# Kernel tuning notes

Measured on AMD Instinct MI355X. Metric: run time of the kernel, lower is better.

Reference implementation:

```python
import jax, jax.numpy as jnp
import numpy as np

BETA = 0.25  # commitment cost


def setup_inputs() -> dict:
    key = jax.random.key(0)
    k1, k2 = jax.random.split(key)
    z = jax.random.normal(k1, (16, 512, 64, 64), dtype=jnp.float32)       # (B, C=e_dim, H, W)
    codebook = jax.random.normal(k2, (1024, 512), dtype=jnp.float32)      # (n_e, e_dim)
    return {"z": z, "codebook": codebook}


def reference(z, codebook):
    b, c, h, w = z.shape
    zp = jnp.transpose(z, (0, 2, 3, 1))                                   # (B, H, W, C)
    zf = zp.reshape(-1, c)                                                # (N, e_dim)

    d = (jnp.sum(zf * zf, axis=1, keepdims=True)
         + jnp.sum(codebook * codebook, axis=1)
         - 2.0 * (zf @ codebook.T))                                       # (N, n_e)
    idx = jnp.argmin(d, axis=1)                                           # (N,)

    # one-hot @ codebook == direct gather
    z_q = codebook[idx].reshape(zp.shape)                                 # (B, H, W, C)

    sg = jax.lax.stop_gradient
    e_latent_loss = jnp.mean((sg(z_q) - zp) ** 2)
    q_latent_loss = jnp.mean((z_q - sg(zp)) ** 2)
    codebook_loss = q_latent_loss + BETA * e_latent_loss

    # straight-through estimator
    z_q_st = zp + sg(z_q - zp)
    z_q_out = jnp.transpose(z_q_st, (0, 3, 1, 2))                         # (B, C, H, W)
    return z_q_out, codebook_loss, idx.reshape(b, 1, h, w)
```

## Files before the change

### kernel.cpp

```cpp
#include <hip/hip_runtime.h>
#include <hip/hip_bf16.h>


typedef _Float16 h8 __attribute__((ext_vector_type(8)));
typedef float f32x16 __attribute__((ext_vector_type(16)));

#define OUT_LOSS  33554432
#define OUT_IDX   33554433
#define MARGIN_T  0.15f

__device__ __forceinline__ void gload_lds16(const void* g, void* l) {
  __builtin_amdgcn_global_load_lds(
      (const __attribute__((address_space(1))) void*)g,
      (__attribute__((address_space(3))) void*)l, 16, 0, 0);
}

__device__ __forceinline__ int zswz(int row) {
  return ((row & 3) << 6) | (((row >> 2) & 3) << 4);
}

__global__ __launch_bounds__(64) void k0_prep(
    const float* __restrict__ cb, unsigned short* __restrict__ cbT,
    float* __restrict__ cnp, int* __restrict__ counters, float* __restrict__ loss_acc,
    int* __restrict__ idx_ws, unsigned long long* __restrict__ packed_ws)
{
  const int r = blockIdx.x, l = threadIdx.x;
  const float* row = cb + (size_t)r * 512;
  float4 a  = *(const float4*)(row + l * 8);
  float4 b4 = *(const float4*)(row + l * 8 + 4);
  h8 hv;
  hv[0] = (_Float16)a.x;  hv[1] = (_Float16)a.y;  hv[2] = (_Float16)a.z;  hv[3] = (_Float16)a.w;
  hv[4] = (_Float16)b4.x; hv[5] = (_Float16)b4.y; hv[6] = (_Float16)b4.z; hv[7] = (_Float16)b4.w;
  {
    const int c  = r >> 5, rr = r & 31;
    const int s  = l >> 1;
    const int hk = l & 1;
    char* dst = reinterpret_cast<char*>(cbT)
              + (size_t)(c * 32 + s) * 1024 + (hk * 32 + rr) * 16;
    *reinterpret_cast<h8*>(dst) = hv;
  }
  float s = a.x*a.x + a.y*a.y + a.z*a.z + a.w*a.w
          + b4.x*b4.x + b4.y*b4.y + b4.z*b4.z + b4.w*b4.w;
  #pragma unroll
  for (int off = 1; off < 64; off <<= 1) s += __shfl_xor(s, off);
  if (l == 0) {
    int jr = r & 31, c = r >> 5;
    int khalf = (jr >> 2) & 1;
    int pat = jr - (khalf << 2);
    int rr2 = (pat & 3) + ((pat >> 3) << 2);
    cnp[(c << 5) + (khalf << 4) + rr2] = 0.5f * s;
  }
  const int pix = (r << 6) + l;
  idx_ws[pix] = (int)0x80000000;
  packed_ws[pix] = ~0ull;
  if (r == 0 && l < 4) counters[l] = 0;
  if (r == 0 && l == 0) *loss_acc = 0.f;
}

__global__ __launch_bounds__(256, 2) void k1_main(
    const float* __restrict__ z, const unsigned short* __restrict__ cbT,
    const float* __restrict__ cnp,
    int* __restrict__ idx_ws, int* __restrict__ flaglist,
    unsigned long long* __restrict__ pairlist, int* __restrict__ counters)
{
  extern __shared__ char smem[];
  float* cn_lds = reinterpret_cast<float*>(smem + 49152);
  const int tid   = threadIdx.x;
  const int lane  = tid & 63;
  const int wave  = tid >> 6;
  const int pxl   = lane & 31;
  const int khalf = lane >> 5;
  const int px0   = blockIdx.x << 7;
  const int b     = px0 >> 12;
  const int hw0   = px0 & 4095;
  const char* cbB = reinterpret_cast<const char*>(cbT);

  h8 bfrag[32];
  for (int i = tid; i < 1024; i += 256) cn_lds[i] = cnp[i];
  #pragma unroll
  for (int p = 0; p < 4; ++p) {
    #pragma unroll
    for (int it2 = 0; it2 < 2; ++it2) {
      const int cg  = tid >> 5;
      const int ch0 = it2 * 64 + cg * 8;
      const int pq  = (tid & 31) * 4;
      const float* src = z + ((size_t)(b * 512 + p * 128 + ch0)) * 4096 + hw0 + pq;
      float4 v[8];
      #pragma unroll
      for (int j = 0; j < 8; ++j) v[j] = *(const float4*)(src + (size_t)j * 4096);
      const float* vf = reinterpret_cast<const float*>(v);
      #pragma unroll
      for (int dp = 0; dp < 4; ++dp) {
        h8 hv;
        #pragma unroll
        for (int j = 0; j < 8; ++j) hv[j] = (_Float16)vf[j * 4 + dp];
        int row = pq + dp;
        int a = (row << 8) + ch0 * 2;
        a ^= zswz(row);
        *reinterpret_cast<h8*>(smem + a) = hv;
      }
    }
    __syncthreads();
    {
      const int row  = (wave << 5) + pxl;
      const int sw   = zswz(row);
      const int base = (row << 8) + (khalf << 4);
      #pragma unroll
      for (int ss = 0; ss < 8; ++ss)
        bfrag[p * 8 + ss] = *reinterpret_cast<const h8*>(smem + ((base + (ss << 5)) ^ sw));
    }
    __syncthreads();
  }

  #pragma unroll
  for (int i = 0; i < 4; ++i)
    gload_lds16(cbB + tid * 16 + i * 4096, smem + tid * 16 + i * 4096);
  #pragma unroll
  for (int i = 0; i < 4; ++i)
    gload_lds16(cbB + 16384 + tid * 16 + i * 4096, smem + 16384 + tid * 16 + i * 4096);
  __syncthreads();

  float v0 = INFINITY, v1 = INFINITY, v2 = INFINITY, v3 = INFINITY;
  int   i0 = 0, i1 = 0, i2 = 0, i3 = 0;
  f32x16 acca, accb;
  #pragma unroll
  for (int i = 0; i < 16; ++i) { acca[i] = 0.f; accb[i] = 0.f; }

  char* p0 = smem;
  char* p1 = smem + 16384;
  char* p2 = smem + 32768;

  for (int c = 0; c < 32; ++c) {
    const bool pf = (c < 31);
    asm volatile("s_waitcnt vmcnt(4)" ::: "memory");
    __builtin_amdgcn_s_barrier();
    __builtin_amdgcn_sched_barrier(0);
    if (pf) {
      const char* src = cbB + (c + 1) * 32768 + tid * 16;
      #pragma unroll
      for (int i = 0; i < 4; ++i)
        gload_lds16(src + i * 4096, p2 + tid * 16 + i * 4096);
    }
    {
      const char* ab = p0 + (khalf << 9) + (pxl << 4);
      h8 f[16];
      #pragma unroll
      for (int q = 0; q < 16; ++q) f[q] = *reinterpret_cast<const h8*>(ab + (q << 10));
      __builtin_amdgcn_s_setprio(1);
      #pragma unroll
      for (int q = 0; q < 8; ++q) {
        acca = __builtin_amdgcn_mfma_f32_32x32x16_f16(f[q],     bfrag[q],     acca, 0, 0, 0);
        accb = __builtin_amdgcn_mfma_f32_32x32x16_f16(f[q + 8], bfrag[q + 8], accb, 0, 0, 0);
      }
      __builtin_amdgcn_s_setprio(0);
    }
    { char* t = p0; p0 = p1; p1 = p2; p2 = t; }
    if (pf) { asm volatile("s_waitcnt vmcnt(4)" ::: "memory"); }
    else    { asm volatile("s_waitcnt vmcnt(0)" ::: "memory"); }
    __builtin_amdgcn_s_barrier();
    __builtin_amdgcn_sched_barrier(0);
    if (pf) {
      const char* src = cbB + (c + 1) * 32768 + 16384 + tid * 16;
      #pragma unroll
      for (int i = 0; i < 4; ++i)
        gload_lds16(src + i * 4096, p2 + tid * 16 + i * 4096);
    }
    {
      const char* ab = p0 + (khalf << 9) + (pxl << 4);
      h8 f[16];
      #pragma unroll
      for (int q = 0; q < 16; ++q) f[q] = *reinterpret_cast<const h8*>(ab + (q << 10));
      __builtin_amdgcn_s_setprio(1);
      #pragma unroll
      for (int q = 0; q < 8; ++q) {
        acca = __builtin_amdgcn_mfma_f32_32x32x16_f16(f[q],     bfrag[16 + q], acca, 0, 0, 0);
        accb = __builtin_amdgcn_mfma_f32_32x32x16_f16(f[q + 8], bfrag[24 + q], accb, 0, 0, 0);
      }
      __builtin_amdgcn_s_setprio(0);
    }
    { char* t = p0; p0 = p1; p1 = p2; p2 = t; }

    {
      const float* cl = cn_lds + (c << 5) + (khalf << 4);
      float4 q0 = *(const float4*)(cl);     float4 q1 = *(const float4*)(cl + 4);
      float4 q2 = *(const float4*)(cl + 8); float4 q3 = *(const float4*)(cl + 12);
      const float cn[16] = {q0.x,q0.y,q0.z,q0.w, q1.x,q1.y,q1.z,q1.w,
                            q2.x,q2.y,q2.z,q2.w, q3.x,q3.y,q3.z,q3.w};
      float sc[16];
      #pragma unroll
      for (int r = 0; r < 16; ++r) sc[r] = cn[r] - (acca[r] + accb[r]);
      float mn = sc[0];
      #pragma unroll
      for (int r = 1; r < 16; ++r) mn = fminf(mn, sc[r]);
      if (__ballot(mn < v3)) {
        const int jbase = (c << 5) + (khalf << 2);
        #pragma unroll
        for (int r = 0; r < 16; ++r) {
          int j = jbase + ((r & 3) + ((r >> 2) << 3));
          float s = sc[r];
          bool c0 = s < v0, c1 = s < v1, c2 = s < v2, c3 = s < v3;
          v3 = c2 ? v2 : (c3 ? s : v3);  i3 = c2 ? i2 : (c3 ? j : i3);
          v2 = c1 ? v1 : (c2 ? s : v2);  i2 = c1 ? i1 : (c2 ? j : i2);
          v1 = c0 ? v0 : (c1 ? s : v1);  i1 = c0 ? i0 : (c1 ? j : i1);
          v0 = c0 ? s  : v0;             i0 = c0 ? j  : i0;
        }
      }
      #pragma unroll
      for (int i = 0; i < 16; ++i) { acca[i] = 0.f; accb[i] = 0.f; }
    }
  }

  {
    float ow0 = __shfl_xor(v0, 32), ow1 = __shfl_xor(v1, 32),
          ow2 = __shfl_xor(v2, 32), ow3 = __shfl_xor(v3, 32);
    int   oj0 = __shfl_xor(i0, 32), oj1 = __shfl_xor(i1, 32),
          oj2 = __shfl_xor(i2, 32), oj3 = __shfl_xor(i3, 32);
    const float ow[4] = {ow0, ow1, ow2, ow3};
    const int   oj[4] = {oj0, oj1, oj2, oj3};
    #pragma unroll
    for (int k = 0; k < 4; ++k) {
      float ov = ow[k]; int oi = oj[k];
      bool c0 = ov < v0, c1 = ov < v1, c2 = ov < v2, c3 = ov < v3;
      v3 = c2 ? v2 : (c3 ? ov : v3);  i3 = c2 ? i2 : (c3 ? oi : i3);
      v2 = c1 ? v1 : (c2 ? ov : v2);  i2 = c1 ? i1 : (c2 ? oi : i2);
      v1 = c0 ? v0 : (c1 ? ov : v1);  i1 = c0 ? i0 : (c1 ? oi : i1);
      v0 = c0 ? ov : v0;              i0 = c0 ? oi : i0;
    }
  }

  const int pix = px0 + (wave << 5) + lane;
  bool sane = (v0 == v0) && (v3 == v3) && ((unsigned)i0 < 1024u);
  bool unfl = sane && (v1 - v0 >= MARGIN_T);
  bool quad = sane && !unfl && (v3 - v0 >= MARGIN_T);
  bool qpred = (lane < 32) && quad;
  bool fpred = (lane < 32) && !unfl && !quad;
  if (lane < 32) idx_ws[pix] = unfl ? i0 : (int)0x80000000;

  unsigned long long qm = __ballot(qpred);
  if (qm) {
    int leader = __ffsll(qm) - 1;
    int base = 0;
    if (lane == leader) base = atomicAdd(&counters[1], __popcll(qm));
    base = __shfl(base, leader);
    if (qpred) {
      int pos = __popcll(qm & ((1ull << lane) - 1ull));
      pairlist[base + pos] = (unsigned long long)(unsigned)pix
          | ((unsigned long long)(unsigned)i0 << 16)
          | ((unsigned long long)(unsigned)i1 << 26)
          | ((unsigned long long)(unsigned)i2 << 36)
          | ((unsigned long long)(unsigned)i3 << 46);
    }
  }
  unsigned long long fm = __ballot(fpred);
  if (fm) {
    int leader = __ffsll(fm) - 1;
    int base = 0;
    if (lane == leader) base = atomicAdd(&counters[0], __popcll(fm));
    base = __shfl(base, leader);
    if (fpred) {
      int pos = __popcll(fm & ((1ull << lane) - 1ull));
      flaglist[base + pos] = pix;
    }
  }
}

__global__ __launch_bounds__(256) void k2a_quad(
    const float* __restrict__ z, const float* __restrict__ cb,
    const unsigned long long* __restrict__ pairlist, const int* __restrict__ counters,
    int* __restrict__ idx_ws)
{
  const int lane = threadIdx.x & 63;
  const int wid  = (blockIdx.x << 2) + (threadIdx.x >> 6);
  const int nwav = gridDim.x << 2;
  const int nf   = counters[1];
  for (int e = wid; e < nf; e += nwav) {
    unsigned long long pk = pairlist[e];
    int pix = (int)(pk & 0xFFFFull);
    int c0 = (int)((pk >> 16) & 1023ull), c1 = (int)((pk >> 26) & 1023ull);
    int c2 = (int)((pk >> 36) & 1023ull), c3 = (int)((pk >> 46) & 1023ull);
    const float* zp = z + (size_t)(pix >> 12) * 512 * 4096 + (pix & 4095);
    double s0 = 0, s1 = 0, s2 = 0, s3 = 0;
    #pragma unroll
    for (int k = 0; k < 8; ++k) {
      int c = lane + (k << 6);
      double zv2 = 2.0 * (double)zp[(size_t)c * 4096];
      double a;
      a = (double)cb[(size_t)c0 * 512 + c]; s0 = fma(a, a - zv2, s0);
      a = (double)cb[(size_t)c1 * 512 + c]; s1 = fma(a, a - zv2, s1);
      a = (double)cb[(size_t)c2 * 512 + c]; s2 = fma(a, a - zv2, s2);
      a = (double)cb[(size_t)c3 * 512 + c]; s3 = fma(a, a - zv2, s3);
    }
    #pragma unroll
    for (int off = 32; off > 0; off >>= 1) {
      s0 += __shfl_xor(s0, off); s1 += __shfl_xor(s1, off);
      s2 += __shfl_xor(s2, off); s3 += __shfl_xor(s3, off);
    }
    double bv = s0; int bi = c0;
    if (s1 < bv || (s1 == bv && c1 < bi)) { bv = s1; bi = c1; }
    if (s2 < bv || (s2 == bv && c2 < bi)) { bv = s2; bi = c2; }
    if (s3 < bv || (s3 == bv && c3 < bi)) { bv = s3; bi = c3; }
    if (lane == 0) idx_ws[pix] = bi;
  }
}

__global__ __launch_bounds__(256) void k2_rescan(
    const float* __restrict__ z, const float* __restrict__ cb,
    const int* __restrict__ flaglist, const int* __restrict__ counters,
    unsigned long long* __restrict__ packed_ws)
{
  __shared__ float zb[16][512];
  __shared__ unsigned long long best[16];
  __shared__ int pixl[16];
  const int t = threadIdx.x;
  const int nflag = counters[0];
  const int ntasks = ((nflag + 15) >> 4) << 2;
  for (int task = blockIdx.x; task < ntasks; task += gridDim.x) {
    const int g = task >> 2, q = task & 3;
    int rem = nflag - (g << 4);
    const int npx = rem < 16 ? rem : 16;
    if (t < 16) {
      best[t] = ~0ull;
      pixl[t] = (t < npx) ? flaglist[(g << 4) + t] : 0;
    }
    __syncthreads();
    for (int i = t; i < (npx << 9); i += 256) {
      int p = i >> 9, c = i & 511;
      int pix = pixl[p];
      zb[p][c] = z[((size_t)(pix >> 12) * 512 + c) * 4096 + (pix & 4095)];
    }
    __syncthreads();
    const int j = (q << 8) + t;
    const float* row = cb + (size_t)j * 512;
    double dot[16];
    #pragma unroll
    for (int p = 0; p < 16; ++p) dot[p] = 0.0;
    double cn = 0.0;
    for (int k = 0; k < 512; k += 4) {
      float4 cv = *(const float4*)(row + k);
      double c0 = cv.x, c1 = cv.y, c2 = cv.z, c3 = cv.w;
      cn = fma(c0, c0, cn); cn = fma(c1, c1, cn);
      cn = fma(c2, c2, cn); cn = fma(c3, c3, cn);
      #pragma unroll
      for (int p = 0; p < 16; ++p) {
        dot[p] = fma(c0, (double)zb[p][k + 0], dot[p]);
        dot[p] = fma(c1, (double)zb[p][k + 1], dot[p]);
        dot[p] = fma(c2, (double)zb[p][k + 2], dot[p]);
        dot[p] = fma(c3, (double)zb[p][k + 3], dot[p]);
      }
    }
    #pragma unroll
    for (int p = 0; p < 16; ++p) {
      if (p < npx) {
        double d = fma(-2.0, dot[p], cn);
        unsigned long long u = (unsigned long long)__double_as_longlong(d);
        u = (u >> 63) ? ~u : (u | 0x8000000000000000ull);
        unsigned long long pkk = (u & ~1023ull) | (unsigned long long)j;
        atomicMin(&best[p], pkk);
      }
    }
    __syncthreads();
    if (t < npx) atomicMin(&packed_ws[pixl[t]], best[t]);
    __syncthreads();
  }
}

__global__ __launch_bounds__(256) void k3_out(
    const float* __restrict__ z, const float* __restrict__ cb,
    const int* __restrict__ idx_ws, const unsigned long long* __restrict__ packed_ws,
    float* __restrict__ out, float* __restrict__ loss_acc)
{
  extern __shared__ float rows[];
  __shared__ int idxs[32];
  __shared__ float wsum[4];
  const int t = threadIdx.x;
  const int pix0 = blockIdx.x << 5;
  const int b = pix0 >> 12, hw0 = pix0 & 4095;
  if (t < 32) {
    int pix = pix0 + t;
    int v = idx_ws[pix];
    unsigned j = (v < 0) ? (unsigned)(packed_ws[pix] & 1023ull) : (unsigned)v;
    j &= 1023u;
    idxs[t] = (int)j;
    out[OUT_IDX + pix] = (float)j;
  }
  __syncthreads();
  for (int i = t; i < 32 * 128; i += 256) {
    int r = i >> 7, kq = (i & 127) << 2;
    float4 v = *(const float4*)(cb + (size_t)idxs[r] * 512 + kq);
    float* dst = rows + r * 513 + kq;
    dst[0] = v.x; dst[1] = v.y; dst[2] = v.z; dst[3] = v.w;
  }
  __syncthreads();
  const int pl = (t & 7) << 2;
  const int cg = t >> 3;
  float acc = 0.f;
  for (int c0 = 0; c0 < 512; c0 += 32) {
    int c = c0 + cg;
    size_t go = ((size_t)(b * 512 + c)) * 4096 + hw0 + pl;
    float4 zv = *(const float4*)(z + go);
    float q0 = rows[(pl + 0) * 513 + c], q1 = rows[(pl + 1) * 513 + c];
    float q2 = rows[(pl + 2) * 513 + c], q3 = rows[(pl + 3) * 513 + c];
    float d0 = q0 - zv.x, d1 = q1 - zv.y, d2 = q2 - zv.z, d3 = q3 - zv.w;
    acc = fmaf(d0, d0, acc); acc = fmaf(d1, d1, acc);
    acc = fmaf(d2, d2, acc); acc = fmaf(d3, d3, acc);
    float4 qv;
    qv.x = zv.x + d0; qv.y = zv.y + d1;
    qv.z = zv.z + d2; qv.w = zv.w + d3;
    *reinterpret_cast<float4*>(out + go) = qv;
  }
  #pragma unroll
  for (int off = 32; off > 0; off >>= 1) acc += __shfl_down(acc, off);
  if ((t & 63) == 0) wsum[t >> 6] = acc;
  __syncthreads();
  if (t == 0) atomicAdd(loss_acc, wsum[0] + wsum[1] + wsum[2] + wsum[3]);
}

__global__ void k4_loss(const float* __restrict__ loss_acc, float* __restrict__ out)
{
  if (threadIdx.x == 0 && blockIdx.x == 0)
    out[OUT_LOSS] = loss_acc[0] * (1.25f / 33554432.f);
}

extern "C" void kernel_launch(void* const* d_in, const int* in_sizes, int n_in,
                              void* d_out, int out_size, void* d_ws, size_t ws_size,
                              hipStream_t stream) {
  const float* z  = (const float*)d_in[0];
  const float* cb = (const float*)d_in[1];
  float* out = (float*)d_out;
  char* ws = (char*)d_ws;
  unsigned short*      cbT       = (unsigned short*)(ws);
  float*               cnp       = (float*)(ws + 1048576);
  int*                 idx_ws    = (int*)(ws + 1052672);
  unsigned long long*  packed_ws = (unsigned long long*)(ws + 1314816);
  int*                 flaglist  = (int*)(ws + 1839104);
  unsigned long long*  pairlist  = (unsigned long long*)(ws + 2095360);
  int*                 counters  = (int*)(ws + 2619648);
  float*               loss_acc  = (float*)(ws + 2619712);

  (void)hipFuncSetAttribute((const void*)k1_main,
        hipFuncAttributeMaxDynamicSharedMemorySize, 53248);
  (void)hipFuncSetAttribute((const void*)k3_out,
        hipFuncAttributeMaxDynamicSharedMemorySize, 65664);

  k0_prep<<<1024, 64, 0, stream>>>(cb, cbT, cnp, counters, loss_acc, idx_ws, packed_ws);
  k1_main<<<512, 256, 53248, stream>>>(z, cbT, cnp, idx_ws, flaglist, pairlist, counters);
  k2a_quad<<<1024, 256, 0, stream>>>(z, cb, pairlist, counters, idx_ws);
  k2_rescan<<<256, 256, 0, stream>>>(z, cb, flaglist, counters, packed_ws);
  k3_out<<<2048, 256, 65664, stream>>>(z, cb, idx_ws, packed_ws, out, loss_acc);
  k4_loss<<<1, 1, 0, stream>>>(loss_acc, out);
}
```

Before: 177.9 us.

## Split codebook search across two blocks per pixel tile with a merge kernel

```diff
diff --git a/kernel.cpp b/kernel.cpp
--- a/kernel.cpp
+++ b/kernel.cpp
@@ -7,7 +7,10 @@
 
 #define OUT_LOSS  33554432
 #define OUT_IDX   33554433
-#define MARGIN_T  0.15f
+#define MARGIN_T  0.17f
+#define FLAG_CAP  32768
+
+struct ull2 { unsigned long long lo, hi; };
 
 __device__ __forceinline__ void gload_lds16(const void* g, void* l) {
   __builtin_amdgcn_global_load_lds(
@@ -19,10 +22,14 @@
   return ((row & 3) << 6) | (((row >> 2) & 3) << 4);
 }
 
+__device__ __forceinline__ float embed(float v, int idx) {
+  unsigned u = (__float_as_uint(v) & ~1023u) | (unsigned)idx;
+  return __uint_as_float(u);
+}
+
 __global__ __launch_bounds__(64) void k0_prep(
     const float* __restrict__ cb, unsigned short* __restrict__ cbT,
-    float* __restrict__ cnp, int* __restrict__ counters, float* __restrict__ loss_acc,
-    int* __restrict__ idx_ws, unsigned long long* __restrict__ packed_ws)
+    float* __restrict__ cnp, int* __restrict__ counters, float* __restrict__ loss_acc)
 {
   const int r = blockIdx.x, l = threadIdx.x;
   const float* row = cb + (size_t)r * 512;
@@ -50,18 +57,13 @@
     int rr2 = (pat & 3) + ((pat >> 3) << 2);
     cnp[(c << 5) + (khalf << 4) + rr2] = 0.5f * s;
   }
-  const int pix = (r << 6) + l;
-  idx_ws[pix] = (int)0x80000000;
-  packed_ws[pix] = ~0ull;
   if (r == 0 && l < 4) counters[l] = 0;
   if (r == 0 && l == 0) *loss_acc = 0.f;
 }
 
 __global__ __launch_bounds__(256, 2) void k1_main(
     const float* __restrict__ z, const unsigned short* __restrict__ cbT,
-    const float* __restrict__ cnp,
-    int* __restrict__ idx_ws, int* __restrict__ flaglist,
-    unsigned long long* __restrict__ pairlist, int* __restrict__ counters)
+    const float* __restrict__ cnp, float4* __restrict__ partial)
 {
   extern __shared__ char smem[];
   float* cn_lds = reinterpret_cast<float*>(smem + 49152);
@@ -70,13 +72,16 @@
   const int wave  = tid >> 6;
   const int pxl   = lane & 31;
   const int khalf = lane >> 5;
-  const int px0   = blockIdx.x << 7;
+  const int bid   = blockIdx.x;
+  const int pxg   = bid >> 1;
+  const int hc    = bid & 1;
+  const int px0   = pxg << 7;
   const int b     = px0 >> 12;
   const int hw0   = px0 & 4095;
-  const char* cbB = reinterpret_cast<const char*>(cbT);
+  const char* cbH = reinterpret_cast<const char*>(cbT) + hc * 524288;
 
   h8 bfrag[32];
-  for (int i = tid; i < 1024; i += 256) cn_lds[i] = cnp[i];
+  for (int i = tid; i < 512; i += 256) cn_lds[i] = cnp[hc * 512 + i];
   #pragma unroll
   for (int p = 0; p < 4; ++p) {
     #pragma unroll
@@ -114,10 +119,10 @@
 
   #pragma unroll
   for (int i = 0; i < 4; ++i)
-    gload_lds16(cbB + tid * 16 + i * 4096, smem + tid * 16 + i * 4096);
+    gload_lds16(cbH + tid * 16 + i * 4096, smem + tid * 16 + i * 4096);
   #pragma unroll
   for (int i = 0; i < 4; ++i)
-    gload_lds16(cbB + 16384 + tid * 16 + i * 4096, smem + 16384 + tid * 16 + i * 4096);
+    gload_lds16(cbH + 16384 + tid * 16 + i * 4096, smem + 16384 + tid * 16 + i * 4096);
   __syncthreads();
 
   float v0 = INFINITY, v1 = INFINITY, v2 = INFINITY, v3 = INFINITY;
@@ -126,17 +131,15 @@
   #pragma unroll
   for (int i = 0; i < 16; ++i) { acca[i] = 0.f; accb[i] = 0.f; }
 
-  char* p0 = smem;
-  char* p1 = smem + 16384;
-  char* p2 = smem + 32768;
-
-  for (int c = 0; c < 32; ++c) {
-    const bool pf = (c < 31);
+  char* p0 = smem; char* p1 = smem + 16384; char* p2 = smem + 32768;
+
+  for (int c = 0; c < 16; ++c) {
+    const bool pf = (c < 15);
     asm volatile("s_waitcnt vmcnt(4)" ::: "memory");
     __builtin_amdgcn_s_barrier();
     __builtin_amdgcn_sched_barrier(0);
     if (pf) {
-      const char* src = cbB + (c + 1) * 32768 + tid * 16;
+      const char* src = cbH + (c + 1) * 32768 + tid * 16;
       #pragma unroll
       for (int i = 0; i < 4; ++i)
         gload_lds16(src + i * 4096, p2 + tid * 16 + i * 4096);
@@ -160,7 +163,7 @@
     __builtin_amdgcn_s_barrier();
     __builtin_amdgcn_sched_barrier(0);
     if (pf) {
-      const char* src = cbB + (c + 1) * 32768 + 16384 + tid * 16;
+      const char* src = cbH + (c + 1) * 32768 + 16384 + tid * 16;
       #pragma unroll
       for (int i = 0; i < 4; ++i)
         gload_lds16(src + i * 4096, p2 + tid * 16 + i * 4096);
@@ -193,7 +196,7 @@
       #pragma unroll
       for (int r = 1; r < 16; ++r) mn = fminf(mn, sc[r]);
       if (__ballot(mn < v3)) {
-        const int jbase = (c << 5) + (khalf << 2);
+        const int jbase = hc * 512 + (c << 5) + (khalf << 2);
         #pragma unroll
         for (int r = 0; r < 16; ++r) {
           int j = jbase + ((r & 3) + ((r >> 2) << 3));
@@ -228,45 +231,85 @@
     }
   }
 
-  const int pix = px0 + (wave << 5) + lane;
-  bool sane = (v0 == v0) && (v3 == v3) && ((unsigned)i0 < 1024u);
-  bool unfl = sane && (v1 - v0 >= MARGIN_T);
-  bool quad = sane && !unfl && (v3 - v0 >= MARGIN_T);
-  bool qpred = (lane < 32) && quad;
-  bool fpred = (lane < 32) && !unfl && !quad;
-  if (lane < 32) idx_ws[pix] = unfl ? i0 : (int)0x80000000;
-
-  unsigned long long qm = __ballot(qpred);
+  if (lane < 32) {
+    const int pix = px0 + (wave << 5) + lane;
+    float4 e;
+    e.x = embed(v0, i0); e.y = embed(v1, i1);
+    e.z = embed(v2, i2); e.w = embed(v3, i3);
+    partial[hc * 65536 + pix] = e;
+  }
+}
+
+__global__ __launch_bounds__(256) void k1_merge(
+    const float4* __restrict__ partial,
+    int* __restrict__ idx_ws, unsigned long long* __restrict__ packed_ws,
+    int* __restrict__ flaglist, ull2* __restrict__ pairlist, int* __restrict__ counters)
+{
+  const int pix  = blockIdx.x * 256 + threadIdx.x;
+  const int lane = threadIdx.x & 63;
+  float4 A = partial[pix], B = partial[65536 + pix];
+  const float cv[8] = {A.x, A.y, A.z, A.w, B.x, B.y, B.z, B.w};
+  int id[8];
+  #pragma unroll
+  for (int j = 0; j < 8; ++j) id[j] = (int)(__float_as_uint(cv[j]) & 1023u);
+
+  float w0 = INFINITY, w1 = INFINITY, w2 = INFINITY, w3 = INFINITY;
+  int   j0 = 0;
+  #pragma unroll
+  for (int k = 0; k < 8; ++k) {
+    float v = cv[k];
+    bool c0 = v < w0, c1 = v < w1, c2 = v < w2, c3 = v < w3;
+    w3 = c2 ? w2 : (c3 ? v : w3);
+    w2 = c1 ? w1 : (c2 ? v : w2);
+    w1 = c0 ? w0 : (c1 ? v : w1);
+    if (c0) { w0 = v; j0 = id[k]; }
+  }
+  float cert = fminf(A.w, B.w);
+  bool sane = (w0 == w0) && (w1 == w1) && (cert == cert);
+  bool unfl = sane && (w1 - w0 >= MARGIN_T);
+  bool oct  = sane && !unfl && (cert - w0 >= MARGIN_T);
+  bool full = !unfl && !oct;
+  idx_ws[pix] = unfl ? j0 : (int)0x80000000;
+  if (!unfl) packed_ws[pix] = ~0ull;
+
+  unsigned long long qm = __ballot(oct);
   if (qm) {
     int leader = __ffsll(qm) - 1;
     int base = 0;
     if (lane == leader) base = atomicAdd(&counters[1], __popcll(qm));
     base = __shfl(base, leader);
-    if (qpred) {
+    if (oct) {
       int pos = __popcll(qm & ((1ull << lane) - 1ull));
-      pairlist[base + pos] = (unsigned long long)(unsigned)pix
-          | ((unsigned long long)(unsigned)i0 << 16)
-          | ((unsigned long long)(unsigned)i1 << 26)
-          | ((unsigned long long)(unsigned)i2 << 36)
-          | ((unsigned long long)(unsigned)i3 << 46);
-    }
-  }
-  unsigned long long fm = __ballot(fpred);
+      ull2 e;
+      e.lo = (unsigned long long)(unsigned)pix
+           | ((unsigned long long)(unsigned)id[0] << 16)
+           | ((unsigned long long)(unsigned)id[1] << 26)
+           | ((unsigned long long)(unsigned)id[2] << 36)
+           | ((unsigned long long)(unsigned)id[3] << 46);
+      e.hi = (unsigned long long)(unsigned)id[4]
+           | ((unsigned long long)(unsigned)id[5] << 10)
+           | ((unsigned long long)(unsigned)id[6] << 20)
+           | ((unsigned long long)(unsigned)id[7] << 30);
+      pairlist[base + pos] = e;
+    }
+  }
+  unsigned long long fm = __ballot(full);
   if (fm) {
     int leader = __ffsll(fm) - 1;
     int base = 0;
     if (lane == leader) base = atomicAdd(&counters[0], __popcll(fm));
     base = __shfl(base, leader);
-    if (fpred) {
+    if (full) {
       int pos = __popcll(fm & ((1ull << lane) - 1ull));
-      flaglist[base + pos] = pix;
-    }
-  }
-}
-
-__global__ __launch_bounds__(256) void k2a_quad(
+      int wi = base + pos;
+      if (wi < FLAG_CAP) flaglist[wi] = pix;
+    }
+  }
+}
+
+__global__ __launch_bounds__(256) void k2a_oct(
     const float* __restrict__ z, const float* __restrict__ cb,
-    const unsigned long long* __restrict__ pairlist, const int* __restrict__ counters,
+    const ull2* __restrict__ pairlist, const int* __restrict__ counters,
     int* __restrict__ idx_ws)
 {
   const int lane = threadIdx.x & 63;
@@ -274,31 +317,37 @@
   const int nwav = gridDim.x << 2;
   const int nf   = counters[1];
   for (int e = wid; e < nf; e += nwav) {
-    unsigned long long pk = pairlist[e];
-    int pix = (int)(pk & 0xFFFFull);
-    int c0 = (int)((pk >> 16) & 1023ull), c1 = (int)((pk >> 26) & 1023ull);
-    int c2 = (int)((pk >> 36) & 1023ull), c3 = (int)((pk >> 46) & 1023ull);
+    ull2 pk = pairlist[e];
+    int pix = (int)(pk.lo & 0xFFFFull);
+    int cd[8];
+    cd[0] = (int)((pk.lo >> 16) & 1023ull); cd[1] = (int)((pk.lo >> 26) & 1023ull);
+    cd[2] = (int)((pk.lo >> 36) & 1023ull); cd[3] = (int)((pk.lo >> 46) & 1023ull);
+    cd[4] = (int)(pk.hi & 1023ull);         cd[5] = (int)((pk.hi >> 10) & 1023ull);
+    cd[6] = (int)((pk.hi >> 20) & 1023ull); cd[7] = (int)((pk.hi >> 30) & 1023ull);
     const float* zp = z + (size_t)(pix >> 12) * 512 * 4096 + (pix & 4095);
-    double s0 = 0, s1 = 0, s2 = 0, s3 = 0;
+    double s[8];
+    #pragma unroll
+    for (int j = 0; j < 8; ++j) s[j] = 0.0;
     #pragma unroll
     for (int k = 0; k < 8; ++k) {
       int c = lane + (k << 6);
       double zv2 = 2.0 * (double)zp[(size_t)c * 4096];
-      double a;
-      a = (double)cb[(size_t)c0 * 512 + c]; s0 = fma(a, a - zv2, s0);
-      a = (double)cb[(size_t)c1 * 512 + c]; s1 = fma(a, a - zv2, s1);
-      a = (double)cb[(size_t)c2 * 512 + c]; s2 = fma(a, a - zv2, s2);
-      a = (double)cb[(size_t)c3 * 512 + c]; s3 = fma(a, a - zv2, s3);
-    }
-    #pragma unroll
-    for (int off = 32; off > 0; off >>= 1) {
-      s0 += __shfl_xor(s0, off); s1 += __shfl_xor(s1, off);
-      s2 += __shfl_xor(s2, off); s3 += __shfl_xor(s3, off);
-    }
-    double bv = s0; int bi = c0;
-    if (s1 < bv || (s1 == bv && c1 < bi)) { bv = s1; bi = c1; }
-    if (s2 < bv || (s2 == bv && c2 < bi)) { bv = s2; bi = c2; }
-    if (s3 < bv || (s3 == bv && c3 < bi)) { bv = s3; bi = c3; }
+      #pragma unroll
+      for (int j = 0; j < 8; ++j) {
+        double a = (double)cb[(size_t)cd[j] * 512 + c];
+        s[j] = fma(a, a - zv2, s[j]);
+      }
+    }
+    #pragma unroll
+    for (int j = 0; j < 8; ++j) {
+      #pragma unroll
+      for (int off = 32; off > 0; off >>= 1) s[j] += __shfl_xor(s[j], off);
+    }
+    double bv = s[0]; int bi = cd[0];
+    #pragma unroll
+    for (int j = 1; j < 8; ++j) {
+      if (s[j] < bv || (s[j] == bv && cd[j] < bi)) { bv = s[j]; bi = cd[j]; }
+    }
     if (lane == 0) idx_ws[pix] = bi;
   }
 }
@@ -312,7 +361,8 @@
   __shared__ unsigned long long best[16];
   __shared__ int pixl[16];
   const int t = threadIdx.x;
-  const int nflag = counters[0];
+  int nflag = counters[0];
+  if (nflag > FLAG_CAP) nflag = FLAG_CAP;
   const int ntasks = ((nflag + 15) >> 4) << 2;
   for (int task = blockIdx.x; task < ntasks; task += gridDim.x) {
     const int g = task >> 2, q = task & 3;
@@ -429,22 +479,24 @@
   float* out = (float*)d_out;
   char* ws = (char*)d_ws;
   unsigned short*      cbT       = (unsigned short*)(ws);
-  float*               cnp       = (float*)(ws + 1048576);
-  int*                 idx_ws    = (int*)(ws + 1052672);
-  unsigned long long*  packed_ws = (unsigned long long*)(ws + 1314816);
-  int*                 flaglist  = (int*)(ws + 1839104);
-  unsigned long long*  pairlist  = (unsigned long long*)(ws + 2095360);
-  int*                 counters  = (int*)(ws + 2619648);
-  float*               loss_acc  = (float*)(ws + 2619712);
+  ull2*                pairlist  = (ull2*)(ws);
+  float4*              partial   = (float4*)(ws + 1048576);
+  int*                 idx_ws    = (int*)(ws + 3145728);
+  unsigned long long*  packed_ws = (unsigned long long*)(ws + 3407872);
+  int*                 flaglist  = (int*)(ws + 3932160);
+  float*               cnp       = (float*)(ws + 4063232);
+  int*                 counters  = (int*)(ws + 4067328);
+  float*               loss_acc  = (float*)(ws + 4067392);
 
   (void)hipFuncSetAttribute((const void*)k1_main,
-        hipFuncAttributeMaxDynamicSharedMemorySize, 53248);
+        hipFuncAttributeMaxDynamicSharedMemorySize, 51200);
   (void)hipFuncSetAttribute((const void*)k3_out,
         hipFuncAttributeMaxDynamicSharedMemorySize, 65664);
 
-  k0_prep<<<1024, 64, 0, stream>>>(cb, cbT, cnp, counters, loss_acc, idx_ws, packed_ws);
-  k1_main<<<512, 256, 53248, stream>>>(z, cbT, cnp, idx_ws, flaglist, pairlist, counters);
-  k2a_quad<<<1024, 256, 0, stream>>>(z, cb, pairlist, counters, idx_ws);
+  k0_prep<<<1024, 64, 0, stream>>>(cb, cbT, cnp, counters, loss_acc);
+  k1_main<<<1024, 256, 51200, stream>>>(z, cbT, cnp, partial);
+  k1_merge<<<256, 256, 0, stream>>>(partial, idx_ws, packed_ws, flaglist, pairlist, counters);
+  k2a_oct<<<512, 256, 0, stream>>>(z, cb, pairlist, counters, idx_ws);
   k2_rescan<<<256, 256, 0, stream>>>(z, cb, flaglist, counters, packed_ws);
   k3_out<<<2048, 256, 65664, stream>>>(z, cb, idx_ws, packed_ws, out, loss_acc);
   k4_loss<<<1, 1, 0, stream>>>(loss_acc, out);
```

Result: slower. 195.7 us (+10.0%).

## Split K across wave pairs in main VQ kernel, halving pixels per block

Applied to the files above, without the earlier changes.

```diff
diff --git a/kernel.cpp b/kernel.cpp
--- a/kernel.cpp
+++ b/kernel.cpp
@@ -32,11 +32,12 @@
   hv[0] = (_Float16)a.x;  hv[1] = (_Float16)a.y;  hv[2] = (_Float16)a.z;  hv[3] = (_Float16)a.w;
   hv[4] = (_Float16)b4.x; hv[5] = (_Float16)b4.y; hv[6] = (_Float16)b4.z; hv[7] = (_Float16)b4.w;
   {
-    const int c  = r >> 5, rr = r & 31;
-    const int s  = l >> 1;
-    const int hk = l & 1;
+    const int c   = r >> 5, rr = r & 31;
+    const int sub = l >> 4;
+    const int s   = (l >> 1) & 7;
+    const int hk  = l & 1;
     char* dst = reinterpret_cast<char*>(cbT)
-              + (size_t)(c * 32 + s) * 1024 + (hk * 32 + rr) * 16;
+              + (size_t)(c * 4 + sub) * 8192 + s * 1024 + (hk * 32 + rr) * 16;
     *reinterpret_cast<h8*>(dst) = hv;
   }
   float s = a.x*a.x + a.y*a.y + a.z*a.z + a.w*a.w
@@ -57,33 +58,42 @@
   if (r == 0 && l == 0) *loss_acc = 0.f;
 }
 
-__global__ __launch_bounds__(256, 2) void k1_main(
+__global__ __launch_bounds__(256, 3) void k1_main(
     const float* __restrict__ z, const unsigned short* __restrict__ cbT,
     const float* __restrict__ cnp,
     int* __restrict__ idx_ws, int* __restrict__ flaglist,
     unsigned long long* __restrict__ pairlist, int* __restrict__ counters)
 {
   extern __shared__ char smem[];
-  float* cn_lds = reinterpret_cast<float*>(smem + 49152);
+  char*  exch   = smem + 24576;
+  float* cn_lds = reinterpret_cast<float*>(smem + 40960);
   const int tid   = threadIdx.x;
   const int lane  = tid & 63;
   const int wave  = tid >> 6;
+  const int pxg   = wave & 1;
+  const int kh    = wave >> 1;
   const int pxl   = lane & 31;
   const int khalf = lane >> 5;
-  const int px0   = blockIdx.x << 7;
+  const int px0   = blockIdx.x << 6;
   const int b     = px0 >> 12;
   const int hw0   = px0 & 4095;
   const char* cbB = reinterpret_cast<const char*>(cbT);
 
-  h8 bfrag[32];
+  #pragma unroll
+  for (int i = 0; i < 2; ++i)
+    gload_lds16(cbB + tid * 16 + i * 4096, smem + tid * 16 + i * 4096);
+  #pragma unroll
+  for (int i = 0; i < 2; ++i)
+    gload_lds16(cbB + 8192 + tid * 16 + i * 4096, smem + 8192 + tid * 16 + i * 4096);
+
+  h8 bfrag[16];
   for (int i = tid; i < 1024; i += 256) cn_lds[i] = cnp[i];
   #pragma unroll
   for (int p = 0; p < 4; ++p) {
-    #pragma unroll
-    for (int it2 = 0; it2 < 2; ++it2) {
-      const int cg  = tid >> 5;
-      const int ch0 = it2 * 64 + cg * 8;
-      const int pq  = (tid & 31) * 4;
+    {
+      const int cg  = tid >> 4;
+      const int ch0 = cg * 8;
+      const int pq  = (tid & 15) * 4;
       const float* src = z + ((size_t)(b * 512 + p * 128 + ch0)) * 4096 + hw0 + pq;
       float4 v[8];
       #pragma unroll
@@ -95,30 +105,22 @@
         #pragma unroll
         for (int j = 0; j < 8; ++j) hv[j] = (_Float16)vf[j * 4 + dp];
         int row = pq + dp;
-        int a = (row << 8) + ch0 * 2;
-        a ^= zswz(row);
-        *reinterpret_cast<h8*>(smem + a) = hv;
+        int a = ((row << 8) + ch0 * 2) ^ zswz(row);
+        *reinterpret_cast<h8*>(exch + a) = hv;
       }
     }
     __syncthreads();
-    {
-      const int row  = (wave << 5) + pxl;
+    if ((p >> 1) == kh) {
+      const int row  = (pxg << 5) + pxl;
       const int sw   = zswz(row);
       const int base = (row << 8) + (khalf << 4);
       #pragma unroll
       for (int ss = 0; ss < 8; ++ss)
-        bfrag[p * 8 + ss] = *reinterpret_cast<const h8*>(smem + ((base + (ss << 5)) ^ sw));
+        bfrag[(p & 1) * 8 + ss] =
+            *reinterpret_cast<const h8*>(exch + ((base + (ss << 5)) ^ sw));
     }
     __syncthreads();
   }
-
-  #pragma unroll
-  for (int i = 0; i < 4; ++i)
-    gload_lds16(cbB + tid * 16 + i * 4096, smem + tid * 16 + i * 4096);
-  #pragma unroll
-  for (int i = 0; i < 4; ++i)
-    gload_lds16(cbB + 16384 + tid * 16 + i * 4096, smem + 16384 + tid * 16 + i * 4096);
-  __syncthreads();
 
   float v0 = INFINITY, v1 = INFINITY, v2 = INFINITY, v3 = INFINITY;
   int   i0 = 0, i1 = 0, i2 = 0, i3 = 0;
@@ -127,139 +129,188 @@
   for (int i = 0; i < 16; ++i) { acca[i] = 0.f; accb[i] = 0.f; }
 
   char* p0 = smem;
-  char* p1 = smem + 16384;
-  char* p2 = smem + 32768;
+  char* p1 = smem + 8192;
+  char* p2 = smem + 16384;
+  const bool mine0 = (kh == 0), mine1 = (kh == 1);
 
   for (int c = 0; c < 32; ++c) {
-    const bool pf = (c < 31);
-    asm volatile("s_waitcnt vmcnt(4)" ::: "memory");
-    __builtin_amdgcn_s_barrier();
-    __builtin_amdgcn_sched_barrier(0);
-    if (pf) {
-      const char* src = cbB + (c + 1) * 32768 + tid * 16;
+    const int stb = c << 2;
+    #pragma unroll
+    for (int sub = 0; sub < 4; ++sub) {
+      const int st = stb + sub;
+      if (st != 127) { asm volatile("s_waitcnt vmcnt(2)" ::: "memory"); }
+      else           { asm volatile("s_waitcnt vmcnt(0)" ::: "memory"); }
+      __builtin_amdgcn_s_barrier();
+      __builtin_amdgcn_sched_barrier(0);
+
+      if (sub == 0 && c > 0 && kh == 0) {
+        const float* exb = reinterpret_cast<const float*>(
+            exch + (((c - 1) & 1) << 13) + (pxg << 12) + lane * 64);
+        float4 e0 = *(const float4*)(exb);
+        float4 e1 = *(const float4*)(exb + 4);
+        float4 e2 = *(const float4*)(exb + 8);
+        float4 e3 = *(const float4*)(exb + 12);
+        const float ex[16] = {e0.x,e0.y,e0.z,e0.w, e1.x,e1.y,e1.z,e1.w,
+                              e2.x,e2.y,e2.z,e2.w, e3.x,e3.y,e3.z,e3.w};
+        const int cc = c - 1;
+        const float* cl = cn_lds + (cc << 5) + (khalf << 4);
+        float4 q0 = *(const float4*)(cl);     float4 q1 = *(const float4*)(cl + 4);
+        float4 q2 = *(const float4*)(cl + 8); float4 q3 = *(const float4*)(cl + 12);
+        const float cn[16] = {q0.x,q0.y,q0.z,q0.w, q1.x,q1.y,q1.z,q1.w,
+                              q2.x,q2.y,q2.z,q2.w, q3.x,q3.y,q3.z,q3.w};
+        float sc[16];
+        #pragma unroll
+        for (int r = 0; r < 16; ++r) sc[r] = cn[r] - (acca[r] + accb[r] + ex[r]);
+        float mn = sc[0];
+        #pragma unroll
+        for (int r = 1; r < 16; ++r) mn = fminf(mn, sc[r]);
+        if (__ballot(mn < v3)) {
+          const int jbase = (cc << 5) + (khalf << 2);
+          #pragma unroll
+          for (int r = 0; r < 16; ++r) {
+            int j = jbase + ((r & 3) + ((r >> 2) << 3));
+            float s = sc[r];
+            bool c0 = s < v0, c1 = s < v1, c2 = s < v2, c3 = s < v3;
+            v3 = c2 ? v2 : (c3 ? s : v3);  i3 = c2 ? i2 : (c3 ? j : i3);
+            v2 = c1 ? v1 : (c2 ? s : v2);  i2 = c1 ? i1 : (c2 ? j : i2);
+            v1 = c0 ? v0 : (c1 ? s : v1);  i1 = c0 ? i0 : (c1 ? j : i1);
+            v0 = c0 ? s  : v0;             i0 = c0 ? j  : i0;
+          }
+        }
+        #pragma unroll
+        for (int i = 0; i < 16; ++i) { acca[i] = 0.f; accb[i] = 0.f; }
+      }
+
+      if (st + 2 < 128) {
+        const char* src = cbB + (size_t)(st + 2) * 8192 + tid * 16;
+        gload_lds16(src,        p2 + tid * 16);
+        gload_lds16(src + 4096, p2 + tid * 16 + 4096);
+      }
+
+      const bool mine = (sub < 2) ? mine0 : mine1;
+      if (mine) {
+        const char* ab = p0 + (khalf << 9) + (pxl << 4);
+        h8 f[8];
+        #pragma unroll
+        for (int q = 0; q < 8; ++q) f[q] = *reinterpret_cast<const h8*>(ab + (q << 10));
+        __builtin_amdgcn_s_setprio(1);
+        #pragma unroll
+        for (int q = 0; q < 4; ++q) {
+          acca = __builtin_amdgcn_mfma_f32_32x32x16_f16(f[q],     bfrag[(sub & 1) * 8 + q],     acca, 0, 0, 0);
+          accb = __builtin_amdgcn_mfma_f32_32x32x16_f16(f[q + 4], bfrag[(sub & 1) * 8 + q + 4], accb, 0, 0, 0);
+        }
+        __builtin_amdgcn_s_setprio(0);
+      }
+
+      if (sub == 3 && kh == 1) {
+        float* exw = reinterpret_cast<float*>(
+            exch + ((c & 1) << 13) + (pxg << 12) + lane * 64);
+        float4 w0, w1, w2, w3;
+        w0.x = acca[0]  + accb[0];  w0.y = acca[1]  + accb[1];
+        w0.z = acca[2]  + accb[2];  w0.w = acca[3]  + accb[3];
+        w1.x = acca[4]  + accb[4];  w1.y = acca[5]  + accb[5];
+        w1.z = acca[6]  + accb[6];  w1.w = acca[7]  + accb[7];
+        w2.x = acca[8]  + accb[8];  w2.y = acca[9]  + accb[9];
+        w2.z = acca[10] + accb[10]; w2.w = acca[11] + accb[11];
+        w3.x = acca[12] + accb[12]; w3.y = acca[13] + accb[13];
+        w3.z = acca[14] + accb[14]; w3.w = acca[15] + accb[15];
+        *(float4*)(exw)      = w0;  *(float4*)(exw + 4)  = w1;
+        *(float4*)(exw + 8)  = w2;  *(float4*)(exw + 12) = w3;
+        asm volatile("s_waitcnt lgkmcnt(0)" ::: "memory");
+        #pragma unroll
+        for (int i = 0; i < 16; ++i) { acca[i] = 0.f; accb[i] = 0.f; }
+      }
+
+      { char* t = p0; p0 = p1; p1 = p2; p2 = t; }
+    }
+  }
+
+  __builtin_amdgcn_s_barrier();
+  if (kh == 0) {
+    const float* exb = reinterpret_cast<const float*>(
+        exch + ((31 & 1) << 13) + (pxg << 12) + lane * 64);
+    float4 e0 = *(const float4*)(exb);
+    float4 e1 = *(const float4*)(exb + 4);
+    float4 e2 = *(const float4*)(exb + 8);
+    float4 e3 = *(const float4*)(exb + 12);
+    const float ex[16] = {e0.x,e0.y,e0.z,e0.w, e1.x,e1.y,e1.z,e1.w,
+                          e2.x,e2.y,e2.z,e2.w, e3.x,e3.y,e3.z,e3.w};
+    const float* cl = cn_lds + (31 << 5) + (khalf << 4);
+    float4 q0 = *(const float4*)(cl);     float4 q1 = *(const float4*)(cl + 4);
+    float4 q2 = *(const float4*)(cl + 8); float4 q3 = *(const float4*)(cl + 12);
+    const float cn[16] = {q0.x,q0.y,q0.z,q0.w, q1.x,q1.y,q1.z,q1.w,
+                          q2.x,q2.y,q2.z,q2.w, q3.x,q3.y,q3.z,q3.w};
+    float sc[16];
+    #pragma unroll
+    for (int r = 0; r < 16; ++r) sc[r] = cn[r] - (acca[r] + accb[r] + ex[r]);
+    float mn = sc[0];
+    #pragma unroll
+    for (int r = 1; r < 16; ++r) mn = fminf(mn, sc[r]);
+    if (__ballot(mn < v3)) {
+      const int jbase = (31 << 5) + (khalf << 2);
       #pragma unroll
-      for (int i = 0; i < 4; ++i)
-        gload_lds16(src + i * 4096, p2 + tid * 16 + i * 4096);
-    }
+      for (int r = 0; r < 16; ++r) {
+        int j = jbase + ((r & 3) + ((r >> 2) << 3));
+        float s = sc[r];
+        bool c0 = s < v0, c1 = s < v1, c2 = s < v2, c3 = s < v3;
+        v3 = c2 ? v2 : (c3 ? s : v3);  i3 = c2 ? i2 : (c3 ? j : i3);
+        v2 = c1 ? v1 : (c2 ? s : v2);  i2 = c1 ? i1 : (c2 ? j : i2);
+        v1 = c0 ? v0 : (c1 ? s : v1);  i1 = c0 ? i0 : (c1 ? j : i1);
+        v0 = c0 ? s  : v0;             i0 = c0 ? j  : i0;
+      }
+    }
+
     {
-      const char* ab = p0 + (khalf << 9) + (pxl << 4);
-      h8 f[16];
+      float ow0 = __shfl_xor(v0, 32), ow1 = __shfl_xor(v1, 32),
+            ow2 = __shfl_xor(v2, 32), ow3 = __shfl_xor(v3, 32);
+      int   oj0 = __shfl_xor(i0, 32), oj1 = __shfl_xor(i1, 32),
+            oj2 = __shfl_xor(i2, 32), oj3 = __shfl_xor(i3, 32);
+      const float ow[4] = {ow0, ow1, ow2, ow3};
+      const int   oj[4] = {oj0, oj1, oj2, oj3};
       #pragma unroll
-      for (int q = 0; q < 16; ++q) f[q] = *reinterpret_cast<const h8*>(ab + (q << 10));
-      __builtin_amdgcn_s_setprio(1);
-      #pragma unroll
-      for (int q = 0; q < 8; ++q) {
-        acca = __builtin_amdgcn_mfma_f32_32x32x16_f16(f[q],     bfrag[q],     acca, 0, 0, 0);
-        accb = __builtin_amdgcn_mfma_f32_32x32x16_f16(f[q + 8], bfrag[q + 8], accb, 0, 0, 0);
-      }
-      __builtin_amdgcn_s_setprio(0);
-    }
-    { char* t = p0; p0 = p1; p1 = p2; p2 = t; }
-    if (pf) { asm volatile("s_waitcnt vmcnt(4)" ::: "memory"); }
-    else    { asm volatile("s_waitcnt vmcnt(0)" ::: "memory"); }
-    __builtin_amdgcn_s_barrier();
-    __builtin_amdgcn_sched_barrier(0);
-    if (pf) {
-      const char* src = cbB + (c + 1) * 32768 + 16384 + tid * 16;
-      #pragma unroll
-      for (int i = 0; i < 4; ++i)
-        gload_lds16(src + i * 4096, p2 + tid * 16 + i * 4096);
-    }
-    {
-      const char* ab = p0 + (khalf << 9) + (pxl << 4);
-      h8 f[16];
-      #pragma unroll
-      for (int q = 0; q < 16; ++q) f[q] = *reinterpret_cast<const h8*>(ab + (q << 10));
-      __builtin_amdgcn_s_setprio(1);
-      #pragma unroll
-      for (int q = 0; q < 8; ++q) {
-        acca = __builtin_amdgcn_mfma_f32_32x32x16_f16(f[q],     bfrag[16 + q], acca, 0, 0, 0);
-        accb = __builtin_amdgcn_mfma_f32_32x32x16_f16(f[q + 8], bfrag[24 + q], accb, 0, 0, 0);
-      }
-      __builtin_amdgcn_s_setprio(0);
-    }
-    { char* t = p0; p0 = p1; p1 = p2; p2 = t; }
-
-    {
-      const float* cl = cn_lds + (c << 5) + (khalf << 4);
-      float4 q0 = *(const float4*)(cl);     float4 q1 = *(const float4*)(cl + 4);
-      float4 q2 = *(const float4*)(cl + 8); float4 q3 = *(const float4*)(cl + 12);
-      const float cn[16] = {q0.x,q0.y,q0.z,q0.w, q1.x,q1.y,q1.z,q1.w,
-                            q2.x,q2.y,q2.z,q2.w, q3.x,q3.y,q3.z,q3.w};
-      float sc[16];
-      #pragma unroll
-      for (int r = 0; r < 16; ++r) sc[r] = cn[r] - (acca[r] + accb[r]);
-      float mn = sc[0];
-      #pragma unroll
-      for (int r = 1; r < 16; ++r) mn = fminf(mn, sc[r]);
-      if (__ballot(mn < v3)) {
-        const int jbase = (c << 5) + (khalf << 2);
-        #pragma unroll
-        for (int r = 0; r < 16; ++r) {
-          int j = jbase + ((r & 3) + ((r >> 2) << 3));
-          float s = sc[r];
-          bool c0 = s < v0, c1 = s < v1, c2 = s < v2, c3 = s < v3;
-          v3 = c2 ? v2 : (c3 ? s : v3);  i3 = c2 ? i2 : (c3 ? j : i3);
-          v2 = c1 ? v1 : (c2 ? s : v2);  i2 = c1 ? i1 : (c2 ? j : i2);
-          v1 = c0 ? v0 : (c1 ? s : v1);  i1 = c0 ? i0 : (c1 ? j : i1);
-          v0 = c0 ? s  : v0;             i0 = c0 ? j  : i0;
-        }
-      }
-      #pragma unroll
-      for (int i = 0; i < 16; ++i) { acca[i] = 0.f; accb[i] = 0.f; }
-    }
-  }
-
-  {
-    float ow0 = __shfl_xor(v0, 32), ow1 = __shfl_xor(v1, 32),
-          ow2 = __shfl_xor(v2, 32), ow3 = __shfl_xor(v3, 32);
-    int   oj0 = __shfl_xor(i0, 32), oj1 = __shfl_xor(i1, 32),
-          oj2 = __shfl_xor(i2, 32), oj3 = __shfl_xor(i3, 32);
-    const float ow[4] = {ow0, ow1, ow2, ow3};
-    const int   oj[4] = {oj0, oj1, oj2, oj3};
-    #pragma unroll
-    for (int k = 0; k < 4; ++k) {
-      float ov = ow[k]; int oi = oj[k];
-      bool c0 = ov < v0, c1 = ov < v1, c2 = ov < v2, c3 = ov < v3;
-      v3 = c2 ? v2 : (c3 ? ov : v3);  i3 = c2 ? i2 : (c3 ? oi : i3);
-      v2 = c1 ? v1 : (c2 ? ov : v2);  i2 = c1 ? i1 : (c2 ? oi : i2);
-      v1 = c0 ? v0 : (c1 ? ov : v1);  i1 = c0 ? i0 : (c1 ? oi : i1);
-      v0 = c0 ? ov : v0;              i0 = c0 ? oi : i0;
-    }
-  }
-
-  const int pix = px0 + (wave << 5) + lane;
-  bool sane = (v0 == v0) && (v3 == v3) && ((unsigned)i0 < 1024u);
-  bool unfl = sane && (v1 - v0 >= MARGIN_T);
-  bool quad = sane && !unfl && (v3 - v0 >= MARGIN_T);
-  bool qpred = (lane < 32) && quad;
-  bool fpred = (lane < 32) && !unfl && !quad;
-  if (lane < 32) idx_ws[pix] = unfl ? i0 : (int)0x80000000;
-
-  unsigned long long qm = __ballot(qpred);
-  if (qm) {
-    int leader = __ffsll(qm) - 1;
-    int base = 0;
-    if (lane == leader) base = atomicAdd(&counters[1], __popcll(qm));
-    base = __shfl(base, leader);
-    if (qpred) {
-      int pos = __popcll(qm & ((1ull << lane) - 1ull));
-      pairlist[base + pos] = (unsigned long long)(unsigned)pix
-          | ((unsigned long long)(unsigned)i0 << 16)
-          | ((unsigned long long)(unsigned)i1 << 26)
-          | ((unsigned long long)(unsigned)i2 << 36)
-          | ((unsigned long long)(unsigned)i3 << 46);
-    }
-  }
-  unsigned long long fm = __ballot(fpred);
-  if (fm) {
-    int leader = __ffsll(fm) - 1;
-    int base = 0;
-    if (lane == leader) base = atomicAdd(&counters[0], __popcll(fm));
-    base = __shfl(base, leader);
-    if (fpred) {
-      int pos = __popcll(fm & ((1ull << lane) - 1ull));
-      flaglist[base + pos] = pix;
+      for (int k = 0; k < 4; ++k) {
+        float ov = ow[k]; int oi = oj[k];
+        bool c0 = ov < v0, c1 = ov < v1, c2 = ov < v2, c3 = ov < v3;
+        v3 = c2 ? v2 : (c3 ? ov : v3);  i3 = c2 ? i2 : (c3 ? oi : i3);
+        v2 = c1 ? v1 : (c2 ? ov : v2);  i2 = c1 ? i1 : (c2 ? oi : i2);
+        v1 = c0 ? v0 : (c1 ? ov : v1);  i1 = c0 ? i0 : (c1 ? oi : i1);
+        v0 = c0 ? ov : v0;              i0 = c0 ? oi : i0;
+      }
+    }
+
+    const int pix = px0 + (pxg << 5) + lane;
+    bool sane = (v0 == v0) && (v3 == v3) && ((unsigned)i0 < 1024u);
+    bool unfl = sane && (v1 - v0 >= MARGIN_T);
+    bool quad = sane && !unfl && (v3 - v0 >= MARGIN_T);
+    bool qpred = (lane < 32) && quad;
+    bool fpred = (lane < 32) && !unfl && !quad;
+    if (lane < 32) idx_ws[pix] = unfl ? i0 : (int)0x80000000;
+
+    unsigned long long qm = __ballot(qpred);
+    if (qm) {
+      int leader = __ffsll(qm) - 1;
+      int base = 0;
+      if (lane == leader) base = atomicAdd(&counters[1], __popcll(qm));
+      base = __shfl(base, leader);
+      if (qpred) {
+        int pos = __popcll(qm & ((1ull << lane) - 1ull));
+        pairlist[base + pos] = (unsigned long long)(unsigned)pix
+            | ((unsigned long long)(unsigned)i0 << 16)
+            | ((unsigned long long)(unsigned)i1 << 26)
+            | ((unsigned long long)(unsigned)i2 << 36)
+            | ((unsigned long long)(unsigned)i3 << 46);
+      }
+    }
+    unsigned long long fm = __ballot(fpred);
+    if (fm) {
+      int leader = __ffsll(fm) - 1;
+      int base = 0;
+      if (lane == leader) base = atomicAdd(&counters[0], __popcll(fm));
+      base = __shfl(base, leader);
+      if (fpred) {
+        int pos = __popcll(fm & ((1ull << lane) - 1ull));
+        flaglist[base + pos] = pix;
+      }
     }
   }
 }
@@ -438,12 +489,12 @@
   float*               loss_acc  = (float*)(ws + 2619712);
 
   (void)hipFuncSetAttribute((const void*)k1_main,
-        hipFuncAttributeMaxDynamicSharedMemorySize, 53248);
+        hipFuncAttributeMaxDynamicSharedMemorySize, 45056);
   (void)hipFuncSetAttribute((const void*)k3_out,
         hipFuncAttributeMaxDynamicSharedMemorySize, 65664);
 
   k0_prep<<<1024, 64, 0, stream>>>(cb, cbT, cnp, counters, loss_acc, idx_ws, packed_ws);
-  k1_main<<<512, 256, 53248, stream>>>(z, cbT, cnp, idx_ws, flaglist, pairlist, counters);
+  k1_main<<<1024, 256, 45056, stream>>>(z, cbT, cnp, idx_ws, flaglist, pairlist, counters);
   k2a_quad<<<1024, 256, 0, stream>>>(z, cb, pairlist, counters, idx_ws);
   k2_rescan<<<256, 256, 0, stream>>>(z, cb, flaglist, counters, packed_ws);
   k3_out<<<2048, 256, 65664, stream>>>(z, cb, idx_ws, packed_ws, out, loss_acc);
```

Result: slower. 244.7 us (+37.6%).
